# Kernel optimization log

Hardware: AMD Instinct MI355X
Metric: run time of the kernel (lower is better)

Reference implementation:

```python
import jax, jax.numpy as jnp
import numpy as np

NOTRACK_BOX = jnp.array([-1.0, -1.0, -1.0, -1.0], dtype=jnp.float32)
ROI_SIZE = 7


def make_boxes(key, B, N):
    k1, k2 = jax.random.split(key)
    lo = jax.random.uniform(k1, (B, N, 2)) * 0.5            # (ymin, xmin)
    sz = jax.random.uniform(k2, (B, N, 2)) * 0.45 + 0.05    # box extent
    hi = jnp.minimum(lo + sz, 1.0)
    boxes = jnp.concatenate([lo, hi], axis=-1)               # [B,N,4] ymin,xmin,ymax,xmax
    # mark last 2 slots per batch as empty (NOTRACK_BOX)
    boxes = boxes.at[:, -2:, :].set(-1.0)
    return boxes


def setup_inputs() -> dict:
    key = jax.random.key(0)
    ks = jax.random.split(key, 6)
    B, H, W, N, C, D = 16, 512, 512, 16, 256, 256
    images = jax.random.normal(ks[0], (B, H, W, 3), dtype=jnp.float32)
    bboxes = make_boxes(ks[1], B, N)
    conv_w = jax.random.normal(ks[2], (16, 16, 3, C), dtype=jnp.float32) * 0.05
    conv_b = jnp.zeros((C,), dtype=jnp.float32)
    dense_w = jax.random.normal(ks[3], (C, D), dtype=jnp.float32) * (1.0 / np.sqrt(C))
    dense_b = jnp.zeros((D,), dtype=jnp.float32)
    return {"images": images, "bboxes": bboxes, "conv_w": conv_w,
            "conv_b": conv_b, "dense_w": dense_w, "dense_b": dense_b}


def backbone(images, conv_w, conv_b):
    # stride-16 conv stem: [B,512,512,3] -> [B,32,32,C]
    feat = jax.lax.conv_general_dilated(
        images, conv_w, window_strides=(16, 16), padding="VALID",
        dimension_numbers=("NHWC", "HWIO", "NHWC"))
    return jax.nn.relu(feat + conv_b)


def roi_align(bboxes, feat, size):
    # bboxes: [B,N,4] normalized (ymin,xmin,ymax,xmax); feat: [B,H,W,C]
    B, H, W, C = feat.shape
    ymin, xmin, ymax, xmax = [bboxes[..., i] for i in range(4)]  # each [B,N]
    steps = (jnp.arange(size, dtype=feat.dtype) + 0.5) / size    # [S]
    ys = ymin[..., None] + (ymax - ymin)[..., None] * steps      # [B,N,S]
    xs = xmin[..., None] + (xmax - xmin)[..., None] * steps      # [B,N,S]
    py = ys * H - 0.5
    px = xs * W - 0.5
    y0f = jnp.floor(py); x0f = jnp.floor(px)
    wy = py - y0f; wx = px - x0f                                 # [B,N,S]
    y0 = jnp.clip(y0f.astype(jnp.int32), 0, H - 1)
    y1 = jnp.clip(y0f.astype(jnp.int32) + 1, 0, H - 1)
    x0 = jnp.clip(x0f.astype(jnp.int32), 0, W - 1)
    x1 = jnp.clip(x0f.astype(jnp.int32) + 1, 0, W - 1)
    N, S = y0.shape[1], size
    def grid(yi, xi):  # [B,N,S] x [B,N,S] -> [B,N,S,S] index grids
        return (jnp.broadcast_to(yi[:, :, :, None], (B, N, S, S)),
                jnp.broadcast_to(xi[:, :, None, :], (B, N, S, S)))
    gather = jax.vmap(lambda f, yy, xx: f[yy, xx])  # per-batch fancy gather
    def corner(yi, xi):
        yy, xx = grid(yi, xi)
        return gather(feat, yy, xx)                              # [B,N,S,S,C]
    w00 = ((1 - wy)[:, :, :, None] * (1 - wx)[:, :, None, :])[..., None]
    w01 = ((1 - wy)[:, :, :, None] * wx[:, :, None, :])[..., None]
    w10 = (wy[:, :, :, None] * (1 - wx)[:, :, None, :])[..., None]
    w11 = (wy[:, :, :, None] * wx[:, :, None, :])[..., None]
    return (w00 * corner(y0, x0) + w01 * corner(y0, x1)
            + w10 * corner(y1, x0) + w11 * corner(y1, x1))        # [B,N,S,S,C]


def reference(images, bboxes, conv_w, conv_b, dense_w, dense_b):
    bboxes = jax.lax.stop_gradient(bboxes)
    feat = backbone(images, conv_w, conv_b)                      # [B,32,32,C]
    roi = roi_align(bboxes, feat, ROI_SIZE)                      # [B,N,S,S,C]
    obj = jnp.mean(roi, axis=(-3, -2))                           # [B,N,C] (mean aggregate)
    is_non_empty = jnp.any(bboxes != NOTRACK_BOX, axis=-1, keepdims=True)
    obj = jnp.where(is_non_empty, obj, jnp.zeros_like(obj))
    return obj @ dense_w + dense_b                               # [B,N,D]
```

## Files before the change

### kernel.cpp

```cpp
#include <hip/hip_runtime.h>
#include <hip/hip_bf16.h>

typedef __attribute__((ext_vector_type(8))) short bf16x8;
typedef __attribute__((ext_vector_type(4))) float f32x4;
typedef __attribute__((ext_vector_type(4))) int i32x4;

__device__ inline unsigned int pack_bf2(float a, float b) {
    unsigned int ua = __builtin_bit_cast(unsigned int, a);
    unsigned int ub = __builtin_bit_cast(unsigned int, b);
    ua = (ua + 0x7fffu + ((ua >> 16) & 1u)) >> 16;
    ub = (ub + 0x7fffu + ((ub >> 16) & 1u)) >> 16;
    return (ub << 16) | (ua & 0xffffu);
}

__global__ void pack_w_kernel(const float* __restrict__ conv_w, i32x4* __restrict__ bpack) {
    int t = blockIdx.x * 256 + threadIdx.x;
    int lane = t & 63;
    int g = t >> 6;
    int nt = g / 24, ks = g - nt * 24;
    int k0 = ks * 32 + ((lane >> 4) << 3);
    int n  = nt * 16 + (lane & 15);
    const float* src = conv_w + (size_t)k0 * 256 + n;
    float v[8];
#pragma unroll
    for (int j = 0; j < 8; ++j) v[j] = src[(size_t)j * 256];
    i32x4 o;
    o.x = pack_bf2(v[0], v[1]);
    o.y = pack_bf2(v[2], v[3]);
    o.z = pack_bf2(v[4], v[5]);
    o.w = pack_bf2(v[6], v[7]);
    bpack[t] = o;
}

__global__ __launch_bounds__(512, 4) void conv_kernel(
    const float* __restrict__ images,
    const i32x4* __restrict__ bpack,
    const float* __restrict__ conv_b,
    float* __restrict__ feat) {
    __shared__ short ldsA[2][64 * 200];

    const int tid  = threadIdx.x;
    const int lane = tid & 63;
    const int w    = tid >> 6;
    const int l15  = lane & 15;
    const int lg   = lane >> 4;

    const int work  = (blockIdx.x & 7) * 64 + (blockIdx.x >> 3);
    const int mi    = work >> 1;
    const int nhalf = work & 1;

    const int ss = tid >> 8;
    const int sr = (tid >> 6) & 3;
    const int tc = tid & 63;
    const int gstrip = 2 * mi + ss;
    const float* rowbase = images
        + (size_t)(((gstrip >> 5) << 9) + ((gstrip & 31) << 4) + sr) * 1536 + tc * 4;

    const float bias = conv_b[nhalf * 128 + w * 16 + l15];
    const i32x4* bp = bpack + (size_t)((nhalf * 8 + w) * 24) * 64 + lane;

    bf16x8 breg[12];
    f32x4 acc[4] = {};
    f32x4 st[6];

#pragma unroll
    for (int u = 0; u < 12; ++u)
        breg[u] = __builtin_bit_cast(bf16x8, bp[(size_t)u * 64]);

#pragma unroll
    for (int p = 0; p < 6; ++p) st[p] = *(const f32x4*)(rowbase + p * 256);
#pragma unroll
    for (int p = 0; p < 6; ++p) {
        int fp = tc + 64 * p;
        int j = fp / 12, q = fp - 12 * j;
        int idx = (ss * 32 + j) * 200 + sr * 48 + q * 4;
        int2 v;
        v.x = pack_bf2(st[p].x, st[p].y);
        v.y = pack_bf2(st[p].z, st[p].w);
        *(int2*)(&ldsA[0][idx]) = v;
    }
#pragma unroll
    for (int p = 0; p < 6; ++p) st[p] = *(const f32x4*)(rowbase + 4 * 1536 + p * 256);

    for (int c = 0; c < 4; ++c) {
        __syncthreads();
        const short* bufA = &ldsA[c & 1][0];
#pragma unroll
        for (int s = 0; s < 6; ++s) {
            bf16x8 aF[4];
#pragma unroll
            for (int mt = 0; mt < 4; ++mt)
                aF[mt] = *(const bf16x8*)(&bufA[(mt * 16 + l15) * 200 + s * 32 + lg * 8]);
#pragma unroll
            for (int mt = 0; mt < 4; ++mt)
                acc[mt] = __builtin_amdgcn_mfma_f32_16x16x32_bf16(
                    aF[mt], breg[(c & 1) * 6 + s], acc[mt], 0, 0, 0);
        }
        if (c == 1) {
#pragma unroll
            for (int u = 0; u < 12; ++u)
                breg[u] = __builtin_bit_cast(bf16x8, bp[(size_t)(12 + u) * 64]);
        }
        if (c < 3) {
            short* dstA = &ldsA[(c + 1) & 1][0];
#pragma unroll
            for (int p = 0; p < 6; ++p) {
                int fp = tc + 64 * p;
                int j = fp / 12, q = fp - 12 * j;
                int idx = (ss * 32 + j) * 200 + sr * 48 + q * 4;
                int2 v;
                v.x = pack_bf2(st[p].x, st[p].y);
                v.y = pack_bf2(st[p].z, st[p].w);
                *(int2*)(&dstA[idx]) = v;
            }
            if (c < 2) {
                const float* rb = rowbase + (size_t)(4 * (c + 2)) * 1536;
#pragma unroll
                for (int p = 0; p < 6; ++p) st[p] = *(const f32x4*)(rb + p * 256);
            }
        }
    }

    const int m0 = mi * 64;
    const int ncol = nhalf * 128 + w * 16 + l15;
#pragma unroll
    for (int mt = 0; mt < 4; ++mt)
#pragma unroll
    for (int r = 0; r < 4; ++r) {
        int m = m0 + mt * 16 + lg * 4 + r;
        float v = acc[mt][r] + bias;
        feat[(size_t)m * 256 + ncol] = fmaxf(v, 0.f);
    }
}

__global__ __launch_bounds__(512) void roi_dense_kernel(
    const float* __restrict__ bboxes,
    const float* __restrict__ feat,
    const float* __restrict__ dense_w,
    const float* __restrict__ dense_b,
    float* __restrict__ out) {
    __shared__ int   offs[4][49];
    __shared__ float wts[4][49];
    __shared__ float part[512];
    __shared__ float objv[256];

    const int bn = blockIdx.x;
    const int b  = bn >> 4;
    const int tid = threadIdx.x;

    const float4 box = *(const float4*)(bboxes + (size_t)bn * 4);
    bool empty = (box.x == -1.f) & (box.y == -1.f) & (box.z == -1.f) & (box.w == -1.f);
    if (empty) {
        if (tid < 256) out[(size_t)bn * 256 + tid] = dense_b[tid];
        return;
    }

    if (tid < 49) {
        int sy = tid / 7, sx = tid - sy * 7;
        float py = (box.x + (box.z - box.x) * ((sy + 0.5f) * (1.0f / 7.0f))) * 32.f - 0.5f;
        float px = (box.y + (box.w - box.y) * ((sx + 0.5f) * (1.0f / 7.0f))) * 32.f - 0.5f;
        float y0f = floorf(py), x0f = floorf(px);
        float wy = py - y0f, wx = px - x0f;
        int y0 = min(max((int)y0f, 0), 31);
        int y1 = min(max((int)y0f + 1, 0), 31);
        int x0 = min(max((int)x0f, 0), 31);
        int x1 = min(max((int)x0f + 1, 0), 31);
        offs[0][tid] = (y0 * 32 + x0) * 256;
        offs[1][tid] = (y0 * 32 + x1) * 256;
        offs[2][tid] = (y1 * 32 + x0) * 256;
        offs[3][tid] = (y1 * 32 + x1) * 256;
        wts[0][tid] = (1.f - wy) * (1.f - wx);
        wts[1][tid] = (1.f - wy) * wx;
        wts[2][tid] = wy * (1.f - wx);
        wts[3][tid] = wy * wx;
    }
    __syncthreads();

    const int c = tid & 255, h = tid >> 8;
    const float* fb = feat + (size_t)b * (1024 * 256) + c;
    float accv = 0.f;
    for (int s = h; s < 49; s += 2) {
        accv += wts[0][s] * fb[offs[0][s]];
        accv += wts[1][s] * fb[offs[1][s]];
        accv += wts[2][s] * fb[offs[2][s]];
        accv += wts[3][s] * fb[offs[3][s]];
    }
    part[tid] = accv;
    __syncthreads();
    if (tid < 256) objv[tid] = (part[tid] + part[tid + 256]) * (1.f / 49.f);
    __syncthreads();

    const float* dwp = dense_w + (size_t)(h * 128) * 256 + c;
    float da = 0.f;
#pragma unroll 8
    for (int cc = 0; cc < 128; ++cc) da += objv[h * 128 + cc] * dwp[(size_t)cc * 256];
    part[tid] = da;
    __syncthreads();
    if (tid < 256) out[(size_t)bn * 256 + tid] = part[tid] + part[tid + 256] + dense_b[tid];
}

extern "C" void kernel_launch(void* const* d_in, const int* in_sizes, int n_in,
                              void* d_out, int out_size, void* d_ws, size_t ws_size,
                              hipStream_t stream) {
    const float* images  = (const float*)d_in[0];
    const float* bboxes  = (const float*)d_in[1];
    const float* conv_w  = (const float*)d_in[2];
    const float* conv_b  = (const float*)d_in[3];
    const float* dense_w = (const float*)d_in[4];
    const float* dense_b = (const float*)d_in[5];
    float* out = (float*)d_out;

    char* ws = (char*)d_ws;
    i32x4* bpack = (i32x4*)ws;
    float* feat  = (float*)(ws + 512 * 1024);

    pack_w_kernel<<<96, 256, 0, stream>>>(conv_w, bpack);
    conv_kernel<<<512, 512, 0, stream>>>(images, bpack, conv_b, feat);
    roi_dense_kernel<<<256, 512, 0, stream>>>(bboxes, feat, dense_w, dense_b, out);
}
```

Measured before the change: 39.05 us.

## Retile conv GEMM into 2x4 wave grid with finer K pipelining

The conv GEMM block now arranges its waves as a 2x4 grid, each computing a 32x32 sub-tile, instead of 8 waves each covering all 64 rows for 16 columns. This cuts the A-fragment LDS reads per wave. The K loop is split into 8 smaller chunks with smaller LDS buffers, and B fragments are streamed from global memory into double-buffered registers instead of being held all at once. The aim is to lower register pressure and LDS traffic and to overlap loads with MFMA. The cost is more barriers and more B loads from global memory.

```diff
diff --git a/kernel.cpp b/kernel.cpp
--- a/kernel.cpp
+++ b/kernel.cpp
@@ -37,99 +37,118 @@
     const i32x4* __restrict__ bpack,
     const float* __restrict__ conv_b,
     float* __restrict__ feat) {
-    __shared__ short ldsA[2][64 * 200];
+    __shared__ short ldsA[2][64 * 104];
 
     const int tid  = threadIdx.x;
     const int lane = tid & 63;
     const int w    = tid >> 6;
     const int l15  = lane & 15;
     const int lg   = lane >> 4;
+    const int wr   = w >> 2;
+    const int wc   = w & 3;
 
     const int work  = (blockIdx.x & 7) * 64 + (blockIdx.x >> 3);
     const int mi    = work >> 1;
     const int nhalf = work & 1;
 
     const int ss = tid >> 8;
-    const int sr = (tid >> 6) & 3;
-    const int tc = tid & 63;
+    const int sr = (tid >> 7) & 1;
+    const int tc = tid & 127;
     const int gstrip = 2 * mi + ss;
     const float* rowbase = images
         + (size_t)(((gstrip >> 5) << 9) + ((gstrip & 31) << 4) + sr) * 1536 + tc * 4;
 
-    const float bias = conv_b[nhalf * 128 + w * 16 + l15];
-    const i32x4* bp = bpack + (size_t)((nhalf * 8 + w) * 24) * 64 + lane;
-
-    bf16x8 breg[12];
-    f32x4 acc[4] = {};
-    f32x4 st[6];
-
-#pragma unroll
-    for (int u = 0; u < 12; ++u)
-        breg[u] = __builtin_bit_cast(bf16x8, bp[(size_t)u * 64]);
-
-#pragma unroll
-    for (int p = 0; p < 6; ++p) st[p] = *(const f32x4*)(rowbase + p * 256);
-#pragma unroll
-    for (int p = 0; p < 6; ++p) {
-        int fp = tc + 64 * p;
-        int j = fp / 12, q = fp - 12 * j;
-        int idx = (ss * 32 + j) * 200 + sr * 48 + q * 4;
+    int widx[3];
+#pragma unroll
+    for (int p = 0; p < 3; ++p) {
+        int fp = tc + (p << 7);
+        int j = (fp * 1366) >> 14;
+        int q = fp - 12 * j;
+        widx[p] = (ss * 32 + j) * 104 + sr * 48 + (q << 2);
+    }
+
+    float bias[2];
+#pragma unroll
+    for (int sub = 0; sub < 2; ++sub)
+        bias[sub] = conv_b[nhalf * 128 + wc * 32 + sub * 16 + l15];
+
+    const i32x4* bp = bpack + (size_t)((nhalf * 8 + wc * 2) * 24) * 64 + lane;
+
+    f32x4 acc[2][2] = {};
+    i32x4 Bc[2][3], Bn[2][3];
+    f32x4 st[3];
+
+#pragma unroll
+    for (int p = 0; p < 3; ++p) st[p] = *(const f32x4*)(rowbase + p * 512);
+#pragma unroll
+    for (int sub = 0; sub < 2; ++sub)
+#pragma unroll
+    for (int s = 0; s < 3; ++s)
+        Bc[sub][s] = bp[(size_t)(sub * 24 + s) * 64];
+#pragma unroll
+    for (int p = 0; p < 3; ++p) {
         int2 v;
         v.x = pack_bf2(st[p].x, st[p].y);
         v.y = pack_bf2(st[p].z, st[p].w);
-        *(int2*)(&ldsA[0][idx]) = v;
-    }
-#pragma unroll
-    for (int p = 0; p < 6; ++p) st[p] = *(const f32x4*)(rowbase + 4 * 1536 + p * 256);
-
-    for (int c = 0; c < 4; ++c) {
-        __syncthreads();
+        *(int2*)(&ldsA[0][widx[p]]) = v;
+    }
+    __syncthreads();
+
+#pragma unroll
+    for (int c = 0; c < 8; ++c) {
+        if (c < 7) {
+            const float* rb = rowbase + (size_t)(c + 1) * 3072;
+#pragma unroll
+            for (int p = 0; p < 3; ++p) st[p] = *(const f32x4*)(rb + p * 512);
+#pragma unroll
+            for (int sub = 0; sub < 2; ++sub)
+#pragma unroll
+            for (int s = 0; s < 3; ++s)
+                Bn[sub][s] = bp[(size_t)(sub * 24 + (c + 1) * 3 + s) * 64];
+        }
         const short* bufA = &ldsA[c & 1][0];
 #pragma unroll
-        for (int s = 0; s < 6; ++s) {
-            bf16x8 aF[4];
-#pragma unroll
-            for (int mt = 0; mt < 4; ++mt)
-                aF[mt] = *(const bf16x8*)(&bufA[(mt * 16 + l15) * 200 + s * 32 + lg * 8]);
-#pragma unroll
-            for (int mt = 0; mt < 4; ++mt)
-                acc[mt] = __builtin_amdgcn_mfma_f32_16x16x32_bf16(
-                    aF[mt], breg[(c & 1) * 6 + s], acc[mt], 0, 0, 0);
-        }
-        if (c == 1) {
-#pragma unroll
-            for (int u = 0; u < 12; ++u)
-                breg[u] = __builtin_bit_cast(bf16x8, bp[(size_t)(12 + u) * 64]);
-        }
-        if (c < 3) {
+        for (int s = 0; s < 3; ++s) {
+            bf16x8 aF0 = *(const bf16x8*)(&bufA[(wr * 32 + l15) * 104 + s * 32 + lg * 8]);
+            bf16x8 aF1 = *(const bf16x8*)(&bufA[(wr * 32 + 16 + l15) * 104 + s * 32 + lg * 8]);
+#pragma unroll
+            for (int sub = 0; sub < 2; ++sub) {
+                bf16x8 bF = __builtin_bit_cast(bf16x8, Bc[sub][s]);
+                acc[0][sub] = __builtin_amdgcn_mfma_f32_16x16x32_bf16(aF0, bF, acc[0][sub], 0, 0, 0);
+                acc[1][sub] = __builtin_amdgcn_mfma_f32_16x16x32_bf16(aF1, bF, acc[1][sub], 0, 0, 0);
+            }
+        }
+        if (c < 7) {
             short* dstA = &ldsA[(c + 1) & 1][0];
 #pragma unroll
-            for (int p = 0; p < 6; ++p) {
-                int fp = tc + 64 * p;
-                int j = fp / 12, q = fp - 12 * j;
-                int idx = (ss * 32 + j) * 200 + sr * 48 + q * 4;
+            for (int p = 0; p < 3; ++p) {
                 int2 v;
                 v.x = pack_bf2(st[p].x, st[p].y);
                 v.y = pack_bf2(st[p].z, st[p].w);
-                *(int2*)(&dstA[idx]) = v;
+                *(int2*)(&dstA[widx[p]]) = v;
             }
-            if (c < 2) {
-                const float* rb = rowbase + (size_t)(4 * (c + 2)) * 1536;
-#pragma unroll
-                for (int p = 0; p < 6; ++p) st[p] = *(const f32x4*)(rb + p * 256);
-            }
-        }
-    }
-
-    const int m0 = mi * 64;
-    const int ncol = nhalf * 128 + w * 16 + l15;
-#pragma unroll
-    for (int mt = 0; mt < 4; ++mt)
+        }
+        __syncthreads();
+        if (c < 7) {
+#pragma unroll
+            for (int sub = 0; sub < 2; ++sub)
+#pragma unroll
+            for (int s = 0; s < 3; ++s)
+                Bc[sub][s] = Bn[sub][s];
+        }
+    }
+
+    const int m0 = mi * 64 + wr * 32;
+    const int nc0 = nhalf * 128 + wc * 32;
+#pragma unroll
+    for (int mt = 0; mt < 2; ++mt)
+#pragma unroll
+    for (int sub = 0; sub < 2; ++sub)
 #pragma unroll
     for (int r = 0; r < 4; ++r) {
         int m = m0 + mt * 16 + lg * 4 + r;
-        float v = acc[mt][r] + bias;
-        feat[(size_t)m * 256 + ncol] = fmaxf(v, 0.f);
+        float v = acc[mt][sub][r] + bias[sub];
+        feat[(size_t)m * 256 + nc0 + sub * 16 + l15] = fmaxf(v, 0.f);
     }
 }
 
```

Measured after the change: 38.71 us. About the same (-0.9%).
